# Optimization experiments

Hardware: AMD Instinct MI355X
Metric: run time of the kernel (lower is better)

The kernel has to match this reference:

```python
import jax, jax.numpy as jnp
import numpy as np

B, NIN, L, N, K, NOUT = 4096, 512, 16, 512, 32, 256
TOTAL = NIN + L * N  # 8704 total nodes in the DAG


def setup_inputs() -> dict:
    key = jax.random.key(0)
    ks = jax.random.split(key, 5)
    x = jax.random.normal(ks[0], (B, NIN), jnp.float32)
    W = jax.random.normal(ks[1], (L, N, K), jnp.float32) * 0.2
    b = jax.random.normal(ks[2], (L, N), jnp.float32) * 0.1
    W_out = jax.random.normal(ks[3], (NOUT, K), jnp.float32) * 0.2
    b_out = jax.random.normal(ks[4], (NOUT,), jnp.float32) * 0.1
    rng = np.random.default_rng(0)
    # layer l may only read nodes computed before it (topological validity)
    idx = np.stack([rng.integers(0, NIN + l * N, size=(N, K)) for l in range(L)]).astype(np.int32)
    idx_out = rng.integers(0, TOTAL, size=(NOUT, K)).astype(np.int32)
    return {"x": x, "W": W, "b": b, "W_out": W_out, "b_out": b_out,
            "idx": jnp.asarray(idx), "idx_out": jnp.asarray(idx_out)}


def reference(x, W, b, W_out, b_out, idx, idx_out):
    # buffer of all node activations, filled topologically (out_dict analog)
    buf0 = jnp.zeros((B, TOTAL), x.dtype).at[:, :NIN].set(x)

    def step(carry, layer):
        buf, l = carry
        li, lW, lb = layer
        gathered = buf[:, li]  # [B, N, K] irregular gather of predecessor outputs
        out = jax.nn.sigmoid(jnp.einsum('bnk,nk->bn', gathered, lW) + lb)  # per-node tiny linear + sigmoid
        buf = jax.lax.dynamic_update_slice(buf, out, (0, NIN + l * N))
        return (buf, l + 1), None

    (buf, _), _ = jax.lax.scan(step, (buf0, jnp.int32(0)), (idx, W, b))
    g = buf[:, idx_out]  # [B, NOUT, K]
    return jax.nn.sigmoid(jnp.einsum('bok,ok->bo', g, W_out) + b_out)
```

## Files before the change

### kernel.cpp

```cpp
#include <hip/hip_runtime.h>
#include <hip/hip_fp16.h>
#include <math.h>

#define B     4096
#define NIN   512
#define L     16
#define N     512
#define K     32
#define NOUT  256
#define HID   (L * N)
#define TOTAL (NIN + L * N)
#define BROWS 8
#define BLOCK 512
#define LDS_BYTES (TOTAL * 16)

typedef __attribute__((ext_vector_type(8))) _Float16 h8;
typedef __attribute__((ext_vector_type(8))) unsigned short u16x8;

__device__ __forceinline__ float sigmoidf_fast(float z) {
    return 1.0f / (1.0f + __expf(-z));
}

__global__ void repack_kernel(const float* __restrict__ W,
                              const int*   __restrict__ idx,
                              const float* __restrict__ W_out,
                              const int*   __restrict__ idx_out,
                              _Float16* __restrict__ wh,
                              unsigned short* __restrict__ i16,
                              _Float16* __restrict__ who,
                              unsigned short* __restrict__ io16)
{
    const int n = blockIdx.x * 64 + threadIdx.x;
    const int* ip; const float* wp; _Float16* wo; unsigned short* io; int scale;
    if (n < HID) {
        ip = idx + (size_t)n * K;      wp = W + (size_t)n * K;
        wo = wh + (size_t)n * K;       io = i16 + (size_t)n * K;   scale = 3;
    } else {
        const int m = n - HID;
        ip = idx_out + (size_t)m * K;  wp = W_out + (size_t)m * K;
        wo = who + (size_t)m * K;      io = io16 + (size_t)m * K;  scale = 0;
    }
    const int rot = n & 7;

    int ci[K]; float cw[K];
    {
        const int4*   ip4 = (const int4*)ip;
        const float4* wp4 = (const float4*)wp;
#pragma unroll
        for (int q = 0; q < 8; ++q) {
            const int4   a = ip4[q];
            const float4 f = wp4[q];
            ci[q * 4 + 0] = a.x; ci[q * 4 + 1] = a.y;
            ci[q * 4 + 2] = a.z; ci[q * 4 + 3] = a.w;
            cw[q * 4 + 0] = f.x; cw[q * 4 + 1] = f.y;
            cw[q * 4 + 2] = f.z; cw[q * 4 + 3] = f.w;
        }
    }

    unsigned long long cnt = 0;
    int sl[K];
    unsigned used = 0;
#pragma unroll
    for (int j = 0; j < K; ++j) {
        const int key = ci[j] & 7;
        const int sh  = key << 3;
        const int rank = (int)((cnt >> sh) & 0xff);
        cnt += 1ull << sh;
        if (rank < 4) {
            const int s = ((key - rot) & 7) + (rank << 3);
            sl[j] = s; used |= 1u << s;
        } else {
            sl[j] = -1;
        }
    }
#pragma unroll
    for (int j = 0; j < K; ++j) {
        int s = sl[j];
        if (s < 0) { s = (int)__builtin_ctz(~used); used |= 1u << s; }
        io[s] = (unsigned short)(ci[j] << scale);
        wo[s] = (_Float16)cw[j];
    }
}

#define GATHERS(CI, V, SH)                                                    \
    _Pragma("unroll")                                                         \
    for (int j = 0; j < 8; ++j) {                                             \
        const int c = ((int)(CI)[j]) << (SH);                                 \
        (V)[j] = *(const h8*)((const char*)buf + c);                          \
    }

#define FMA8(V, W8, FA)                                                       \
    {                                                                         \
        h8 a8 = {(_Float16)0.f, (_Float16)0.f, (_Float16)0.f, (_Float16)0.f, \
                 (_Float16)0.f, (_Float16)0.f, (_Float16)0.f, (_Float16)0.f};\
        _Pragma("unroll")                                                     \
        for (int j = 0; j < 8; ++j) {                                         \
            h8 wt;                                                            \
            _Pragma("unroll")                                                 \
            for (int k = 0; k < 8; ++k) wt[k] = (W8)[j];                      \
            a8 = __builtin_elementwise_fma((V)[j], wt, a8);                   \
        }                                                                     \
        _Pragma("unroll")                                                     \
        for (int r = 0; r < 8; ++r) (FA)[r] += (float)a8[r];                  \
    }

#define LAYER(IDXQ, LI, SH)                                                   \
    {                                                                         \
        const h8* wp = (const h8*)(wh + ((size_t)(LI) * N + t) * K);          \
        const h8 w0 = wp[0], w1 = wp[1], w2 = wp[2], w3 = wp[3];              \
        const float bb = bias[(LI) * N + t];                                  \
        h8 v0[8], v1[8], v2[8], v3[8];                                        \
        GATHERS(IDXQ[0], v0, SH)                                              \
        GATHERS(IDXQ[1], v1, SH)                                              \
        GATHERS(IDXQ[2], v2, SH)                                              \
        float fa[8] = {0.f,0.f,0.f,0.f,0.f,0.f,0.f,0.f};                      \
        FMA8(v0, w0, fa)                                                      \
        GATHERS(IDXQ[3], v3, SH)                                              \
        FMA8(v1, w1, fa)                                                      \
        FMA8(v2, w2, fa)                                                      \
        FMA8(v3, w3, fa)                                                      \
        h8 o;                                                                 \
        _Pragma("unroll")                                                     \
        for (int r = 0; r < 8; ++r)                                           \
            o[r] = (_Float16)sigmoidf_fast(fa[r] + bb);                       \
        buf[NIN + (LI) * N + t] = o;                                          \
    }

__global__ __launch_bounds__(BLOCK, 2)
void ffnet_kernel(const float* __restrict__ x,
                  const float* __restrict__ bias,
                  const float* __restrict__ bias_out,
                  const _Float16*       __restrict__ wh,
                  const unsigned short* __restrict__ i16,
                  const _Float16*       __restrict__ who,
                  const unsigned short* __restrict__ io16,
                  float* __restrict__ out)
{
    extern __shared__ h8 buf[];

    const int t  = threadIdx.x;
    const int r0 = blockIdx.x * BROWS;

    {
        h8 v;
#pragma unroll
        for (int r = 0; r < 8; ++r)
            v[r] = (_Float16)x[(size_t)(r0 + r) * NIN + t];
        buf[t] = v;
    }

    u16x8 ia[4], ib[4];
    {
        const u16x8* ip = (const u16x8*)(i16 + (size_t)t * K);
        ia[0] = ip[0]; ia[1] = ip[1]; ia[2] = ip[2]; ia[3] = ip[3];
    }
    __syncthreads();

    for (int l = 0; l < L; l += 2) {
        {
            const u16x8* np = (const u16x8*)(i16 + ((size_t)(l + 1) * N + t) * K);
            ib[0] = np[0]; ib[1] = np[1]; ib[2] = np[2]; ib[3] = np[3];
        }
        LAYER(ia, l, 1)
        __syncthreads();

        if (l + 2 < L) {
            const u16x8* np = (const u16x8*)(i16 + ((size_t)(l + 2) * N + t) * K);
            ia[0] = np[0]; ia[1] = np[1]; ia[2] = np[2]; ia[3] = np[3];
        } else if (t < NOUT) {
            const u16x8* np = (const u16x8*)(io16 + (size_t)t * K);
            ia[0] = np[0]; ia[1] = np[1]; ia[2] = np[2]; ia[3] = np[3];
        }
        LAYER(ib, l + 1, 1)
        __syncthreads();
    }

    if (t < NOUT) {
        const h8* wp = (const h8*)(who + (size_t)t * K);
        const h8 w0 = wp[0], w1 = wp[1], w2 = wp[2], w3 = wp[3];
        const float bb = bias_out[t];

        h8 v0[8], v1[8], v2[8], v3[8];
        GATHERS(ia[0], v0, 4)
        GATHERS(ia[1], v1, 4)
        GATHERS(ia[2], v2, 4)
        float fa[8] = {0.f,0.f,0.f,0.f,0.f,0.f,0.f,0.f};
        FMA8(v0, w0, fa)
        GATHERS(ia[3], v3, 4)
        FMA8(v1, w1, fa)
        FMA8(v2, w2, fa)
        FMA8(v3, w3, fa)

#pragma unroll
        for (int r = 0; r < 8; ++r)
            out[(size_t)(r0 + r) * NOUT + t] = sigmoidf_fast(fa[r] + bb);
    }
}

extern "C" void kernel_launch(void* const* d_in, const int* in_sizes, int n_in,
                              void* d_out, int out_size, void* d_ws, size_t ws_size,
                              hipStream_t stream) {
    const float* x     = (const float*)d_in[0];
    const float* W     = (const float*)d_in[1];
    const float* b     = (const float*)d_in[2];
    const float* W_out = (const float*)d_in[3];
    const float* b_out = (const float*)d_in[4];
    const int*   idx   = (const int*)d_in[5];
    const int*   idx_o = (const int*)d_in[6];
    float* out = (float*)d_out;

    char* ws = (char*)d_ws;
    _Float16*       wh   = (_Float16*)      (ws);
    unsigned short* i16  = (unsigned short*)(ws + 524288);
    _Float16*       who  = (_Float16*)      (ws + 1048576);
    unsigned short* io16 = (unsigned short*)(ws + 1048576 + 16384);

    const int nneur = HID + NOUT;
    repack_kernel<<<dim3(nneur / 64), dim3(64), 0, stream>>>(
        W, idx, W_out, idx_o, wh, i16, who, io16);

    ffnet_kernel<<<dim3(B / BROWS), dim3(BLOCK), LDS_BYTES, stream>>>(
        x, b, b_out, wh, i16, who, io16, out);
}
```

Before: 149.5 us.

## Jointly schedule gather slots across neuron octets; prefetch weights; use half2 FMA structs

The repack kernel now processes eight consecutive neurons per thread and assigns each gather slot so that, at each step, the eight neurons' reads fall in different LDS bank groups. This is meant to reduce LDS bank conflicts among adjacent threads in the main kernel. The main kernel also prefetches the next layer's weights and bias together with its indices. Activations are stored as a struct of half2 pairs so the FMAs map to packed 2-wide operations. The repack now runs a serial 32-step loop per thread with 8x fewer threads, which may lengthen the preprocessing launch.

```diff
diff --git a/kernel.cpp b/kernel.cpp
--- a/kernel.cpp
+++ b/kernel.cpp
@@ -13,72 +13,127 @@
 #define BROWS 8
 #define BLOCK 512
 #define LDS_BYTES (TOTAL * 16)
-
+#define NOCT  ((HID + NOUT) / 8)
+
+typedef __attribute__((ext_vector_type(2))) _Float16 hv2;
 typedef __attribute__((ext_vector_type(8))) _Float16 h8;
 typedef __attribute__((ext_vector_type(8))) unsigned short u16x8;
 
+struct alignas(16) g16 { hv2 p0, p1, p2, p3; };
+
 __device__ __forceinline__ float sigmoidf_fast(float z) {
     return 1.0f / (1.0f + __expf(-z));
 }
 
-__global__ void repack_kernel(const float* __restrict__ W,
-                              const int*   __restrict__ idx,
-                              const float* __restrict__ W_out,
-                              const int*   __restrict__ idx_out,
-                              _Float16* __restrict__ wh,
-                              unsigned short* __restrict__ i16,
-                              _Float16* __restrict__ who,
-                              unsigned short* __restrict__ io16)
+__global__ __launch_bounds__(64)
+void repack_kernel(const float* __restrict__ W,
+                   const int*   __restrict__ idx,
+                   const float* __restrict__ W_out,
+                   const int*   __restrict__ idx_out,
+                   _Float16* __restrict__ wh,
+                   unsigned short* __restrict__ i16,
+                   _Float16* __restrict__ who,
+                   unsigned short* __restrict__ io16)
 {
-    const int n = blockIdx.x * 64 + threadIdx.x;
-    const int* ip; const float* wp; _Float16* wo; unsigned short* io; int scale;
-    if (n < HID) {
-        ip = idx + (size_t)n * K;      wp = W + (size_t)n * K;
-        wo = wh + (size_t)n * K;       io = i16 + (size_t)n * K;   scale = 3;
+    const int oct = blockIdx.x * 64 + threadIdx.x;
+    if (oct >= NOCT) return;
+    const int nb = oct * 8;
+    const int* ibase; const float* wbase; _Float16* wob; unsigned short* iob; int scale;
+    if (nb < HID) {
+        ibase = idx + (size_t)nb * K;      wbase = W + (size_t)nb * K;
+        wob = wh + (size_t)nb * K;         iob = i16 + (size_t)nb * K;   scale = 3;
     } else {
-        const int m = n - HID;
-        ip = idx_out + (size_t)m * K;  wp = W_out + (size_t)m * K;
-        wo = who + (size_t)m * K;      io = io16 + (size_t)m * K;  scale = 0;
-    }
-    const int rot = n & 7;
-
-    int ci[K]; float cw[K];
-    {
-        const int4*   ip4 = (const int4*)ip;
-        const float4* wp4 = (const float4*)wp;
+        const int m = nb - HID;
+        ibase = idx_out + (size_t)m * K;   wbase = W_out + (size_t)m * K;
+        wob = who + (size_t)m * K;         iob = io16 + (size_t)m * K;   scale = 0;
+    }
+
+    unsigned km[8][8];
+    unsigned ne[8];
+#pragma unroll
+    for (int Ln = 0; Ln < 8; ++Ln) {
+        unsigned b0 = 0, b1 = 0, b2 = 0;
+        const int4* ip4 = (const int4*)(ibase + Ln * K);
+#pragma unroll
+        for (int q = 0; q < 8; ++q) {
+            const int4 a = ip4[q];
+            const int j0 = q * 4;
+            b0 |= (unsigned)( a.x       & 1) << (j0 + 0);
+            b1 |= (unsigned)((a.x >> 1) & 1) << (j0 + 0);
+            b2 |= (unsigned)((a.x >> 2) & 1) << (j0 + 0);
+            b0 |= (unsigned)( a.y       & 1) << (j0 + 1);
+            b1 |= (unsigned)((a.y >> 1) & 1) << (j0 + 1);
+            b2 |= (unsigned)((a.y >> 2) & 1) << (j0 + 1);
+            b0 |= (unsigned)( a.z       & 1) << (j0 + 2);
+            b1 |= (unsigned)((a.z >> 1) & 1) << (j0 + 2);
+            b2 |= (unsigned)((a.z >> 2) & 1) << (j0 + 2);
+            b0 |= (unsigned)( a.w       & 1) << (j0 + 3);
+            b1 |= (unsigned)((a.w >> 1) & 1) << (j0 + 3);
+            b2 |= (unsigned)((a.w >> 2) & 1) << (j0 + 3);
+        }
+        unsigned nn = 0;
+#pragma unroll
+        for (int k = 0; k < 8; ++k) {
+            const unsigned m = ((k & 1) ? b0 : ~b0)
+                             & ((k & 2) ? b1 : ~b1)
+                             & ((k & 4) ? b2 : ~b2);
+            km[Ln][k] = m;
+            nn |= (m ? 1u : 0u) << k;
+        }
+        ne[Ln] = nn;
+    }
+
+    unsigned long long sp[8][4];
+#pragma unroll
+    for (int Ln = 0; Ln < 8; ++Ln)
+#pragma unroll
+        for (int h = 0; h < 4; ++h) sp[Ln][h] = 0ull;
+
+    for (int s = 0; s < 32; ++s) {
+        unsigned avail = 0xFFu;
+        const int r = s & 7;
+#pragma unroll
+        for (int Ln = 0; Ln < 8; ++Ln) {
+            const unsigned cand = avail & ne[Ln];
+            const unsigned sel  = cand ? cand : ne[Ln];
+            const unsigned rotsel = ((sel >> r) | (sel << (8 - r))) & 0xFFu;
+            const int k = (__builtin_ctz(rotsel) + r) & 7;
+            unsigned mrow = km[Ln][0];
+#pragma unroll
+            for (int kk = 1; kk < 8; ++kk) mrow = (k == kk) ? km[Ln][kk] : mrow;
+            const int j = __builtin_ctz(mrow);
+            const unsigned mnew = mrow & (mrow - 1);
+#pragma unroll
+            for (int kk = 0; kk < 8; ++kk) km[Ln][kk] = (k == kk) ? mnew : km[Ln][kk];
+            ne[Ln] &= ~(((mnew == 0u) ? 1u : 0u) << k);
+            const unsigned long long wbits =
+                (unsigned long long)(unsigned)s << (6 * (j & 7));
+            const int hi = j >> 3;
+#pragma unroll
+            for (int h = 0; h < 4; ++h) sp[Ln][h] |= (hi == h) ? wbits : 0ull;
+            avail &= ~(1u << k);
+        }
+    }
+
+#pragma unroll
+    for (int Ln = 0; Ln < 8; ++Ln) {
+        const int4*   ip4 = (const int4*)(ibase + Ln * K);
+        const float4* wp4 = (const float4*)(wbase + Ln * K);
+        unsigned short* io = iob + Ln * K;
+        _Float16*       wo = wob + Ln * K;
 #pragma unroll
         for (int q = 0; q < 8; ++q) {
             const int4   a = ip4[q];
             const float4 f = wp4[q];
-            ci[q * 4 + 0] = a.x; ci[q * 4 + 1] = a.y;
-            ci[q * 4 + 2] = a.z; ci[q * 4 + 3] = a.w;
-            cw[q * 4 + 0] = f.x; cw[q * 4 + 1] = f.y;
-            cw[q * 4 + 2] = f.z; cw[q * 4 + 3] = f.w;
-        }
-    }
-
-    unsigned long long cnt = 0;
-    int sl[K];
-    unsigned used = 0;
-#pragma unroll
-    for (int j = 0; j < K; ++j) {
-        const int key = ci[j] & 7;
-        const int sh  = key << 3;
-        const int rank = (int)((cnt >> sh) & 0xff);
-        cnt += 1ull << sh;
-        if (rank < 4) {
-            const int s = ((key - rot) & 7) + (rank << 3);
-            sl[j] = s; used |= 1u << s;
-        } else {
-            sl[j] = -1;
-        }
-    }
-#pragma unroll
-    for (int j = 0; j < K; ++j) {
-        int s = sl[j];
-        if (s < 0) { s = (int)__builtin_ctz(~used); used |= 1u << s; }
-        io[s] = (unsigned short)(ci[j] << scale);
-        wo[s] = (_Float16)cw[j];
+            {   const int j = q*4+0; const int s = (int)((sp[Ln][j>>3] >> (6*(j&7))) & 63u);
+                io[s] = (unsigned short)(a.x << scale); wo[s] = (_Float16)f.x; }
+            {   const int j = q*4+1; const int s = (int)((sp[Ln][j>>3] >> (6*(j&7))) & 63u);
+                io[s] = (unsigned short)(a.y << scale); wo[s] = (_Float16)f.y; }
+            {   const int j = q*4+2; const int s = (int)((sp[Ln][j>>3] >> (6*(j&7))) & 63u);
+                io[s] = (unsigned short)(a.z << scale); wo[s] = (_Float16)f.z; }
+            {   const int j = q*4+3; const int s = (int)((sp[Ln][j>>3] >> (6*(j&7))) & 63u);
+                io[s] = (unsigned short)(a.w << scale); wo[s] = (_Float16)f.w; }
+        }
     }
 }
 
@@ -86,44 +141,49 @@
     _Pragma("unroll")                                                         \
     for (int j = 0; j < 8; ++j) {                                             \
         const int c = ((int)(CI)[j]) << (SH);                                 \
-        (V)[j] = *(const h8*)((const char*)buf + c);                          \
+        (V)[j] = *(const g16*)((const char*)buf + c);                         \
     }
 
 #define FMA8(V, W8, FA)                                                       \
     {                                                                         \
-        h8 a8 = {(_Float16)0.f, (_Float16)0.f, (_Float16)0.f, (_Float16)0.f, \
-                 (_Float16)0.f, (_Float16)0.f, (_Float16)0.f, (_Float16)0.f};\
+        hv2 a0 = {(_Float16)0.f, (_Float16)0.f};                              \
+        hv2 a1 = a0, a2 = a0, a3 = a0;                                        \
         _Pragma("unroll")                                                     \
         for (int j = 0; j < 8; ++j) {                                         \
-            h8 wt;                                                            \
-            _Pragma("unroll")                                                 \
-            for (int k = 0; k < 8; ++k) wt[k] = (W8)[j];                      \
-            a8 = __builtin_elementwise_fma((V)[j], wt, a8);                   \
+            hv2 wt2; wt2.x = (W8)[j]; wt2.y = (W8)[j];                        \
+            a0 = __builtin_elementwise_fma((V)[j].p0, wt2, a0);               \
+            a1 = __builtin_elementwise_fma((V)[j].p1, wt2, a1);               \
+            a2 = __builtin_elementwise_fma((V)[j].p2, wt2, a2);               \
+            a3 = __builtin_elementwise_fma((V)[j].p3, wt2, a3);               \
         }                                                                     \
-        _Pragma("unroll")                                                     \
-        for (int r = 0; r < 8; ++r) (FA)[r] += (float)a8[r];                  \
-    }
-
-#define LAYER(IDXQ, LI, SH)                                                   \
+        (FA)[0] += (float)a0.x;  (FA)[1] += (float)a0.y;                      \
+        (FA)[2] += (float)a1.x;  (FA)[3] += (float)a1.y;                      \
+        (FA)[4] += (float)a2.x;  (FA)[5] += (float)a2.y;                      \
+        (FA)[6] += (float)a3.x;  (FA)[7] += (float)a3.y;                      \
+    }
+
+#define LAYER(IDXQ, WQ0, WQ1, WQ2, WQ3, BB, NOUTIDX)                          \
     {                                                                         \
-        const h8* wp = (const h8*)(wh + ((size_t)(LI) * N + t) * K);          \
-        const h8 w0 = wp[0], w1 = wp[1], w2 = wp[2], w3 = wp[3];              \
-        const float bb = bias[(LI) * N + t];                                  \
-        h8 v0[8], v1[8], v2[8], v3[8];                                        \
-        GATHERS(IDXQ[0], v0, SH)                                              \
-        GATHERS(IDXQ[1], v1, SH)                                              \
-        GATHERS(IDXQ[2], v2, SH)                                              \
+        g16 v0[8], v1[8], v2[8], v3[8];                                       \
+        GATHERS(IDXQ[0], v0, 1)                                               \
+        GATHERS(IDXQ[1], v1, 1)                                               \
+        GATHERS(IDXQ[2], v2, 1)                                               \
         float fa[8] = {0.f,0.f,0.f,0.f,0.f,0.f,0.f,0.f};                      \
-        FMA8(v0, w0, fa)                                                      \
-        GATHERS(IDXQ[3], v3, SH)                                              \
-        FMA8(v1, w1, fa)                                                      \
-        FMA8(v2, w2, fa)                                                      \
-        FMA8(v3, w3, fa)                                                      \
-        h8 o;                                                                 \
-        _Pragma("unroll")                                                     \
-        for (int r = 0; r < 8; ++r)                                           \
-            o[r] = (_Float16)sigmoidf_fast(fa[r] + bb);                       \
-        buf[NIN + (LI) * N + t] = o;                                          \
+        FMA8(v0, WQ0, fa)                                                     \
+        GATHERS(IDXQ[3], v3, 1)                                               \
+        FMA8(v1, WQ1, fa)                                                     \
+        FMA8(v2, WQ2, fa)                                                     \
+        FMA8(v3, WQ3, fa)                                                     \
+        g16 o;                                                                \
+        o.p0.x = (_Float16)sigmoidf_fast(fa[0] + (BB));                       \
+        o.p0.y = (_Float16)sigmoidf_fast(fa[1] + (BB));                       \
+        o.p1.x = (_Float16)sigmoidf_fast(fa[2] + (BB));                       \
+        o.p1.y = (_Float16)sigmoidf_fast(fa[3] + (BB));                       \
+        o.p2.x = (_Float16)sigmoidf_fast(fa[4] + (BB));                       \
+        o.p2.y = (_Float16)sigmoidf_fast(fa[5] + (BB));                       \
+        o.p3.x = (_Float16)sigmoidf_fast(fa[6] + (BB));                       \
+        o.p3.y = (_Float16)sigmoidf_fast(fa[7] + (BB));                       \
+        buf[NIN + (NOUTIDX)] = o;                                             \
     }
 
 __global__ __launch_bounds__(BLOCK, 2)
@@ -136,23 +196,33 @@
                   const unsigned short* __restrict__ io16,
                   float* __restrict__ out)
 {
-    extern __shared__ h8 buf[];
+    extern __shared__ g16 buf[];
 
     const int t  = threadIdx.x;
     const int r0 = blockIdx.x * BROWS;
 
     {
-        h8 v;
-#pragma unroll
-        for (int r = 0; r < 8; ++r)
-            v[r] = (_Float16)x[(size_t)(r0 + r) * NIN + t];
+        g16 v;
+        v.p0.x = (_Float16)x[(size_t)(r0 + 0) * NIN + t];
+        v.p0.y = (_Float16)x[(size_t)(r0 + 1) * NIN + t];
+        v.p1.x = (_Float16)x[(size_t)(r0 + 2) * NIN + t];
+        v.p1.y = (_Float16)x[(size_t)(r0 + 3) * NIN + t];
+        v.p2.x = (_Float16)x[(size_t)(r0 + 4) * NIN + t];
+        v.p2.y = (_Float16)x[(size_t)(r0 + 5) * NIN + t];
+        v.p3.x = (_Float16)x[(size_t)(r0 + 6) * NIN + t];
+        v.p3.y = (_Float16)x[(size_t)(r0 + 7) * NIN + t];
         buf[t] = v;
     }
 
     u16x8 ia[4], ib[4];
+    h8 wa0, wa1, wa2, wa3, wb0, wb1, wb2, wb3;
+    float ba, bb2;
     {
         const u16x8* ip = (const u16x8*)(i16 + (size_t)t * K);
         ia[0] = ip[0]; ia[1] = ip[1]; ia[2] = ip[2]; ia[3] = ip[3];
+        const h8* wp = (const h8*)(wh + (size_t)t * K);
+        wa0 = wp[0]; wa1 = wp[1]; wa2 = wp[2]; wa3 = wp[3];
+        ba = bias[t];
     }
     __syncthreads();
 
@@ -160,40 +230,45 @@
         {
             const u16x8* np = (const u16x8*)(i16 + ((size_t)(l + 1) * N + t) * K);
             ib[0] = np[0]; ib[1] = np[1]; ib[2] = np[2]; ib[3] = np[3];
-        }
-        LAYER(ia, l, 1)
+            const h8* wp = (const h8*)(wh + ((size_t)(l + 1) * N + t) * K);
+            wb0 = wp[0]; wb1 = wp[1]; wb2 = wp[2]; wb3 = wp[3];
+            bb2 = bias[(l + 1) * N + t];
+        }
+        LAYER(ia, wa0, wa1, wa2, wa3, ba, l * N + t)
         __syncthreads();
 
         if (l + 2 < L) {
             const u16x8* np = (const u16x8*)(i16 + ((size_t)(l + 2) * N + t) * K);
             ia[0] = np[0]; ia[1] = np[1]; ia[2] = np[2]; ia[3] = np[3];
+            const h8* wp = (const h8*)(wh + ((size_t)(l + 2) * N + t) * K);
+            wa0 = wp[0]; wa1 = wp[1]; wa2 = wp[2]; wa3 = wp[3];
+            ba = bias[(l + 2) * N + t];
         } else if (t < NOUT) {
             const u16x8* np = (const u16x8*)(io16 + (size_t)t * K);
             ia[0] = np[0]; ia[1] = np[1]; ia[2] = np[2]; ia[3] = np[3];
-        }
-        LAYER(ib, l + 1, 1)
+            const h8* wp = (const h8*)(who + (size_t)t * K);
+            wa0 = wp[0]; wa1 = wp[1]; wa2 = wp[2]; wa3 = wp[3];
+            ba = bias_out[t];
+        }
+        LAYER(ib, wb0, wb1, wb2, wb3, bb2, (l + 1) * N + t)
         __syncthreads();
     }
 
     if (t < NOUT) {
-        const h8* wp = (const h8*)(who + (size_t)t * K);
-        const h8 w0 = wp[0], w1 = wp[1], w2 = wp[2], w3 = wp[3];
-        const float bb = bias_out[t];
-
-        h8 v0[8], v1[8], v2[8], v3[8];
+        g16 v0[8], v1[8], v2[8], v3[8];
         GATHERS(ia[0], v0, 4)
         GATHERS(ia[1], v1, 4)
         GATHERS(ia[2], v2, 4)
         float fa[8] = {0.f,0.f,0.f,0.f,0.f,0.f,0.f,0.f};
-        FMA8(v0, w0, fa)
+        FMA8(v0, wa0, fa)
         GATHERS(ia[3], v3, 4)
-        FMA8(v1, w1, fa)
-        FMA8(v2, w2, fa)
-        FMA8(v3, w3, fa)
-
-#pragma unroll
-        for (int r = 0; r < 8; ++r)
-            out[(size_t)(r0 + r) * NOUT + t] = sigmoidf_fast(fa[r] + bb);
+        FMA8(v1, wa1, fa)
+        FMA8(v2, wa2, fa)
+        FMA8(v3, wa3, fa)
+
+#pragma unroll
+        for (int rr = 0; rr < 8; ++rr)
+            out[(size_t)(r0 + rr) * NOUT + t] = sigmoidf_fast(fa[rr] + ba);
     }
 }
 
@@ -215,8 +290,7 @@
     _Float16*       who  = (_Float16*)      (ws + 1048576);
     unsigned short* io16 = (unsigned short*)(ws + 1048576 + 16384);
 
-    const int nneur = HID + NOUT;
-    repack_kernel<<<dim3(nneur / 64), dim3(64), 0, stream>>>(
+    repack_kernel<<<dim3((NOCT + 63) / 64), dim3(64), 0, stream>>>(
         W, idx, W_out, idx_o, wh, i16, who, io16);
 
     ffnet_kernel<<<dim3(B / BROWS), dim3(BLOCK), LDS_BYTES, stream>>>(
```

New measurement: 205.1 us. +37.2%, slower.
